# Performance work log

Hardware: AMD Instinct MI355X
Metric: run time of the kernel (lower is better)

The kernel has to match this reference:

```python
import jax, jax.numpy as jnp
import numpy as np

B, H, S, D = 2, 16, 2048, 128

def setup_inputs() -> dict:
    key = jax.random.key(0)
    kq, kk, kv = jax.random.split(key, 3)
    q = jax.random.normal(kq, (B, H, S, D), dtype=jnp.float32)
    k = jax.random.normal(kk, (B, H, S, D), dtype=jnp.float32)
    v = jax.random.normal(kv, (B, H, S, D), dtype=jnp.float32)
    # causal mask, broadcastable over batch and heads; 0 -> masked out
    mask = jnp.tril(jnp.ones((S, S), dtype=jnp.int32))[None, None, :, :]
    return {"q": q, "k": k, "v": v, "mask": mask}

def reference(q, k, v, mask):
    # scores: [B,H,S,S] -- note: module applies NO 1/sqrt(d) scaling
    attn = jnp.einsum('bhqd,bhkd->bhqk', q, k)
    neg_inf = jnp.finfo(attn.dtype).min
    attn = jnp.where(mask == 0, neg_inf, attn)
    attn = jax.nn.softmax(attn, axis=-1)
    out = jnp.einsum('bhqk,bhkd->bhqd', attn, v)
    return out
```

## Files before the change

kernel.cpp:

```cpp
#include <hip/hip_runtime.h>


#define SQ 2048
#define DH 128
#define BM 64
#define BN 64
#define NELEM 8388608

typedef _Float16 f16x8 __attribute__((ext_vector_type(8)));
typedef float f32x4 __attribute__((ext_vector_type(4)));
typedef unsigned short u16x8 __attribute__((ext_vector_type(8)));

typedef __attribute__((address_space(3))) void lds_t;
typedef __attribute__((address_space(1))) void gmem_t;

__device__ __forceinline__ void gload16(void* lds, const void* g) {
  __builtin_amdgcn_global_load_lds((const gmem_t*)g, (lds_t*)lds, 16, 0, 0);
}

__device__ __forceinline__ unsigned short f2h(float f) {
  return __builtin_bit_cast(unsigned short, (_Float16)f);
}

__global__ __launch_bounds__(256) void prep(const float* __restrict__ k,
                                            const float* __restrict__ v,
                                            unsigned short* __restrict__ ko,
                                            unsigned short* __restrict__ vt) {
  const int tid = threadIdx.x;
  const int bx = blockIdx.x;
  if (bx < 1024) {
    __shared__ unsigned short lv[64 * 132];
    const int bh = bx >> 5;
    const int s0 = (bx & 31) * 64;
    const float* vs = v + ((size_t)bh * SQ + s0) * DH;
    #pragma unroll
    for (int it = 0; it < 8; ++it) {
      int fi = it * 256 + tid;
      int sL = fi >> 5;
      int dL = (fi & 31) * 4;
      float4 val = *(const float4*)(vs + (size_t)sL * DH + dL);
      ushort4 o;
      o.x = f2h(val.x); o.y = f2h(val.y); o.z = f2h(val.z); o.w = f2h(val.w);
      *(ushort4*)(lv + sL * 132 + dL) = o;
    }
    __syncthreads();
    #pragma unroll
    for (int it = 0; it < 4; ++it) {
      int ci = it * 256 + tid;
      int dL = ci >> 3;
      int sg = ci & 7;
      u16x8 o;
      #pragma unroll
      for (int j = 0; j < 8; ++j) o[j] = lv[(sg * 8 + j) * 132 + dL];
      *(u16x8*)(vt + ((size_t)bh * DH + dL) * SQ + s0 + sg * 8) = o;
    }
  } else {
    const int NT = NELEM / 4;
    for (int i = (bx - 1024) * 256 + tid; i < NT; i += 2048 * 256) {
      float4 val = ((const float4*)k)[i];
      ushort4 o;
      o.x = f2h(val.x); o.y = f2h(val.y); o.z = f2h(val.z); o.w = f2h(val.w);
      ((ushort4*)ko)[i] = o;
    }
  }
}

__global__ __launch_bounds__(256, 2) void fattn(const float* __restrict__ Qf,
                                                const unsigned short* __restrict__ Kh,
                                                const unsigned short* __restrict__ Vth,
                                                float* __restrict__ Out) {
  __shared__ char smem[73728];
  const int tid  = threadIdx.x;
  const int wave = tid >> 6;
  const int lane = tid & 63;
  const int quad = lane >> 4;
  const int c    = lane & 15;

  const int t     = (int)blockIdx.x;
  const int xcd   = t & 7;
  const int idx   = t >> 3;
  const int cu    = idx & 31;
  const int round = idx >> 5;
  const int bh    = xcd * 4 + round;
  int qb;
  {
    int b0 = (cu + 8 * (round >> 1)) & 31;
    qb = (round & 1) ? (31 - b0) : b0;
  }
  const int rowbase = qb * BM;

  char* sP = smem + 65536 + wave * 2048;

  const float* Qg = Qf + ((size_t)bh * SQ + rowbase) * DH;
  #pragma unroll
  for (int it = 0; it < 8; ++it) {
    int gi  = it * 256 + tid;
    int row = gi >> 5;
    int sub = gi & 31;
    float4 qv = *(const float4*)(Qg + (size_t)row * DH + sub * 4);
    ushort4 h;
    h.x = f2h(qv.x); h.y = f2h(qv.y); h.z = f2h(qv.z); h.w = f2h(qv.w);
    int gr = (sub >> 1) ^ (row & 7);
    *(ushort4*)(smem + 32768 + row * 256 + gr * 16 + (sub & 1) * 8) = h;
  }
  __syncthreads();

  const unsigned short* Kbase = Kh + (size_t)bh * SQ * DH;
  const unsigned short* Vbase = Vth + (size_t)bh * DH * SQ;
  const unsigned short* Ksrc = Kbase + (size_t)(tid >> 4) * DH
                             + ((tid & 15) ^ ((tid >> 4) & 7)) * 8;
  const unsigned short* Vsrc = Vbase + (size_t)(tid >> 3) * SQ
                             + ((tid & 7) ^ ((tid >> 3) & 7)) * 8;
  const int ldsbase = wave * 1024;

  #pragma unroll
  for (int it = 0; it < 4; ++it)
    gload16(smem + ldsbase + it * 4096, Ksrc + it * (16 * DH));
  #pragma unroll
  for (int it = 0; it < 4; ++it)
    gload16(smem + 16384 + ldsbase + it * 4096, Vsrc + it * (32 * SQ));

  f16x8 qf[4];
  {
    int rl = wave * 16 + c;
    #pragma unroll
    for (int ch = 0; ch < 4; ++ch) {
      int gr = (ch * 4 + quad) ^ (c & 7);
      qf[ch] = *(const f16x8*)(smem + 32768 + rl * 256 + gr * 16);
    }
  }
  __syncthreads();

  f32x4 acc[8];
  #pragma unroll
  for (int dt = 0; dt < 8; ++dt) acc[dt] = (f32x4){0.f, 0.f, 0.f, 0.f};
  float mo = -1e30f, lrow = 0.f;

  const int nkt = qb + 1;
  int cur = 0;
  for (int kt = 0; kt < nkt; ++kt) {
    char* sK = smem + (cur << 15);
    char* sV = sK + 16384;

    if (kt + 1 < nkt) {
      char* nb = smem + ((cur ^ 1) << 15);
      const unsigned short* Kn = Ksrc + (size_t)(kt + 1) * (BN * DH);
      const unsigned short* Vn = Vsrc + (size_t)(kt + 1) * BN;
      #pragma unroll
      for (int it = 0; it < 4; ++it)
        gload16(nb + ldsbase + it * 4096, Kn + it * (16 * DH));
      #pragma unroll
      for (int it = 0; it < 4; ++it)
        gload16(nb + 16384 + ldsbase + it * 4096, Vn + it * (32 * SQ));
    }

    const bool diag  = (kt == qb);
    const int ntmax  = diag ? wave : 3;
    const int chmax  = diag ? (wave >> 1) : 1;

    f32x4 sc[4];
    #pragma unroll
    for (int nt = 0; nt < 4; ++nt) sc[nt] = (f32x4){0.f, 0.f, 0.f, 0.f};
    __builtin_amdgcn_s_setprio(1);
    #pragma unroll
    for (int nt = 0; nt < 4; ++nt) {
      if (nt <= ntmax) {
        int keyl = nt * 16 + c;
        #pragma unroll
        for (int ch = 0; ch < 4; ++ch) {
          int gr = (ch * 4 + quad) ^ (c & 7);
          f16x8 kf = *(const f16x8*)(sK + keyl * 256 + gr * 16);
          sc[nt] = __builtin_amdgcn_mfma_f32_16x16x32_f16(kf, qf[ch], sc[nt], 0, 0, 0);
        }
      }
    }
    __builtin_amdgcn_s_setprio(0);

    if (diag) {
      int rl = wave * 16 + c;
      #pragma unroll
      for (int nt = 0; nt < 4; ++nt)
        #pragma unroll
        for (int r = 0; r < 4; ++r)
          if (nt * 16 + quad * 4 + r > rl) sc[nt][r] = -1e30f;
    }

    float cm = -1e30f;
    #pragma unroll
    for (int nt = 0; nt < 4; ++nt)
      #pragma unroll
      for (int r = 0; r < 4; ++r) cm = fmaxf(cm, sc[nt][r]);
    cm = fmaxf(cm, __shfl_xor(cm, 16));
    cm = fmaxf(cm, __shfl_xor(cm, 32));
    float mn = fmaxf(mo, cm);
    float al = __expf(mo - mn);
    float rs = 0.f;
    ushort4 pk[4];
    #pragma unroll
    for (int nt = 0; nt < 4; ++nt) {
      #pragma unroll
      for (int r = 0; r < 4; ++r) {
        float p = __expf(sc[nt][r] - mn);
        rs += p;
        ((unsigned short*)&pk[nt])[r] = f2h(p);
      }
    }
    rs += __shfl_xor(rs, 16);
    rs += __shfl_xor(rs, 32);
    lrow = lrow * al + rs;
    mo = mn;
    #pragma unroll
    for (int dt = 0; dt < 8; ++dt) acc[dt] *= al;

    #pragma unroll
    for (int nt = 0; nt < 4; ++nt) {
      int g8 = nt * 2 + (quad >> 1);
      *(ushort4*)(sP + c * 128 + ((g8 ^ (c & 7)) * 16) + (quad & 1) * 8) = pk[nt];
    }

    __builtin_amdgcn_s_setprio(1);
    #pragma unroll
    for (int ch = 0; ch < 2; ++ch) {
      if (ch <= chmax) {
        f16x8 pf = *(const f16x8*)(sP + c * 128 + (((ch * 4 + quad) ^ (c & 7)) * 16));
        #pragma unroll
        for (int dt = 0; dt < 8; ++dt) {
          int d  = dt * 16 + c;
          int gr = (ch * 4 + quad) ^ (c & 7);
          f16x8 vf = *(const f16x8*)(sV + d * 128 + gr * 16);
          acc[dt] = __builtin_amdgcn_mfma_f32_16x16x32_f16(vf, pf, acc[dt], 0, 0, 0);
        }
      }
    }
    __builtin_amdgcn_s_setprio(0);

    if (kt + 1 < nkt) __syncthreads();
    cur ^= 1;
  }

  const float inv = 1.0f / lrow;
  const int rowg = rowbase + wave * 16 + c;
  float* op = Out + ((size_t)bh * SQ + rowg) * DH;
  #pragma unroll
  for (int dt = 0; dt < 8; ++dt) {
    float4 o;
    o.x = acc[dt][0] * inv;
    o.y = acc[dt][1] * inv;
    o.z = acc[dt][2] * inv;
    o.w = acc[dt][3] * inv;
    *(float4*)(op + dt * 16 + quad * 4) = o;
  }
}

extern "C" void kernel_launch(void* const* d_in, const int* in_sizes, int n_in,
                              void* d_out, int out_size, void* d_ws, size_t ws_size,
                              hipStream_t stream) {
  const float* q = (const float*)d_in[0];
  const float* k = (const float*)d_in[1];
  const float* v = (const float*)d_in[2];
  float* out = (float*)d_out;

  unsigned short* kws = (unsigned short*)d_ws;
  unsigned short* vws = kws + NELEM;

  prep<<<3072, 256, 0, stream>>>(k, v, kws, vws);
  fattn<<<1024, 256, 0, stream>>>(q, kws, vws, out);
}
```

Baseline: 225.6 us.

## Replace LDS double-buffered direct loads with register prefetch to raise occupancy

```diff
diff --git a/kernel.cpp b/kernel.cpp
--- a/kernel.cpp
+++ b/kernel.cpp
@@ -10,13 +10,7 @@
 typedef _Float16 f16x8 __attribute__((ext_vector_type(8)));
 typedef float f32x4 __attribute__((ext_vector_type(4)));
 typedef unsigned short u16x8 __attribute__((ext_vector_type(8)));
-
-typedef __attribute__((address_space(3))) void lds_t;
-typedef __attribute__((address_space(1))) void gmem_t;
-
-__device__ __forceinline__ void gload16(void* lds, const void* g) {
-  __builtin_amdgcn_global_load_lds((const gmem_t*)g, (lds_t*)lds, 16, 0, 0);
-}
+typedef unsigned int u32x4 __attribute__((ext_vector_type(4)));
 
 __device__ __forceinline__ unsigned short f2h(float f) {
   return __builtin_bit_cast(unsigned short, (_Float16)f);
@@ -65,11 +59,11 @@
   }
 }
 
-__global__ __launch_bounds__(256, 2) void fattn(const float* __restrict__ Qf,
+__global__ __launch_bounds__(256, 4) void fattn(const float* __restrict__ Qf,
                                                 const unsigned short* __restrict__ Kh,
                                                 const unsigned short* __restrict__ Vth,
                                                 float* __restrict__ Out) {
-  __shared__ char smem[73728];
+  __shared__ char smem[40960];
   const int tid  = threadIdx.x;
   const int wave = tid >> 6;
   const int lane = tid & 63;
@@ -89,7 +83,9 @@
   }
   const int rowbase = qb * BM;
 
-  char* sP = smem + 65536 + wave * 2048;
+  char* sK = smem;
+  char* sV = smem + 16384;
+  char* sP = smem + 32768 + wave * 2048;
 
   const float* Qg = Qf + ((size_t)bh * SQ + rowbase) * DH;
   #pragma unroll
@@ -101,9 +97,18 @@
     ushort4 h;
     h.x = f2h(qv.x); h.y = f2h(qv.y); h.z = f2h(qv.z); h.w = f2h(qv.w);
     int gr = (sub >> 1) ^ (row & 7);
-    *(ushort4*)(smem + 32768 + row * 256 + gr * 16 + (sub & 1) * 8) = h;
+    *(ushort4*)(smem + row * 256 + gr * 16 + (sub & 1) * 8) = h;
   }
   __syncthreads();
+  f16x8 qf[4];
+  {
+    int rl = wave * 16 + c;
+    #pragma unroll
+    for (int ch = 0; ch < 4; ++ch) {
+      int gr = (ch * 4 + quad) ^ (c & 7);
+      qf[ch] = *(const f16x8*)(smem + rl * 256 + gr * 16);
+    }
+  }
 
   const unsigned short* Kbase = Kh + (size_t)bh * SQ * DH;
   const unsigned short* Vbase = Vth + (size_t)bh * DH * SQ;
@@ -111,24 +116,22 @@
                              + ((tid & 15) ^ ((tid >> 4) & 7)) * 8;
   const unsigned short* Vsrc = Vbase + (size_t)(tid >> 3) * SQ
                              + ((tid & 7) ^ ((tid >> 3) & 7)) * 8;
-  const int ldsbase = wave * 1024;
-
-  #pragma unroll
-  for (int it = 0; it < 4; ++it)
-    gload16(smem + ldsbase + it * 4096, Ksrc + it * (16 * DH));
-  #pragma unroll
-  for (int it = 0; it < 4; ++it)
-    gload16(smem + 16384 + ldsbase + it * 4096, Vsrc + it * (32 * SQ));
-
-  f16x8 qf[4];
-  {
-    int rl = wave * 16 + c;
-    #pragma unroll
-    for (int ch = 0; ch < 4; ++ch) {
-      int gr = (ch * 4 + quad) ^ (c & 7);
-      qf[ch] = *(const f16x8*)(smem + 32768 + rl * 256 + gr * 16);
-    }
-  }
+
+  u32x4 kreg[4], vreg[4];
+  #pragma unroll
+  for (int it = 0; it < 4; ++it)
+    kreg[it] = *(const u32x4*)(Ksrc + it * (16 * DH));
+  #pragma unroll
+  for (int it = 0; it < 4; ++it)
+    vreg[it] = *(const u32x4*)(Vsrc + it * (32 * SQ));
+  __syncthreads();
+
+  #pragma unroll
+  for (int it = 0; it < 4; ++it)
+    *(u32x4*)(sK + it * 4096 + tid * 16) = kreg[it];
+  #pragma unroll
+  for (int it = 0; it < 4; ++it)
+    *(u32x4*)(sV + it * 4096 + tid * 16) = vreg[it];
   __syncthreads();
 
   f32x4 acc[8];
@@ -137,22 +140,18 @@
   float mo = -1e30f, lrow = 0.f;
 
   const int nkt = qb + 1;
-  int cur = 0;
   for (int kt = 0; kt < nkt; ++kt) {
-    char* sK = smem + (cur << 15);
-    char* sV = sK + 16384;
-
     if (kt + 1 < nkt) {
-      char* nb = smem + ((cur ^ 1) << 15);
       const unsigned short* Kn = Ksrc + (size_t)(kt + 1) * (BN * DH);
       const unsigned short* Vn = Vsrc + (size_t)(kt + 1) * BN;
       #pragma unroll
       for (int it = 0; it < 4; ++it)
-        gload16(nb + ldsbase + it * 4096, Kn + it * (16 * DH));
-      #pragma unroll
-      for (int it = 0; it < 4; ++it)
-        gload16(nb + 16384 + ldsbase + it * 4096, Vn + it * (32 * SQ));
-    }
+        kreg[it] = *(const u32x4*)(Kn + it * (16 * DH));
+      #pragma unroll
+      for (int it = 0; it < 4; ++it)
+        vreg[it] = *(const u32x4*)(Vn + it * (32 * SQ));
+    }
+    __builtin_amdgcn_sched_barrier(0);
 
     const bool diag  = (kt == qb);
     const int ntmax  = diag ? wave : 3;
@@ -234,8 +233,16 @@
     }
     __builtin_amdgcn_s_setprio(0);
 
-    if (kt + 1 < nkt) __syncthreads();
-    cur ^= 1;
+    if (kt + 1 < nkt) {
+      __syncthreads();
+      #pragma unroll
+      for (int it = 0; it < 4; ++it)
+        *(u32x4*)(sK + it * 4096 + tid * 16) = kreg[it];
+      #pragma unroll
+      for (int it = 0; it < 4; ++it)
+        *(u32x4*)(sV + it * 4096 + tid * 16) = vreg[it];
+      __syncthreads();
+    }
   }
 
   const float inv = 1.0f / lrow;
```

After: 207.9 us. 7.9% less time.
